# Optimization experiments

Measured on AMD Instinct MI355X. Metric: run time of the kernel, lower is better.

## Reference

```python
import jax, jax.numpy as jnp
import numpy as np

B, LQ, LM = 8, 128, 512
Q_SIZE, M_SIZE, H_SIZE = 512, 512, 256
MASKED_VALUE = -1e24


def setup_inputs() -> dict:
    key = jax.random.key(0)
    ks = jax.random.split(key, 8)
    query = jax.random.normal(ks[0], (B, LQ, Q_SIZE), dtype=jnp.float32)
    memory = jax.random.normal(ks[1], (B, LM, M_SIZE), dtype=jnp.float32)
    mask = jax.random.randint(ks[2], (B, LM), 0, 2).astype(bool)
    s_q = 1.0 / np.sqrt(Q_SIZE)
    s_m = 1.0 / np.sqrt(M_SIZE)
    s_h = 1.0 / np.sqrt(H_SIZE)
    Wq = jax.random.uniform(ks[3], (Q_SIZE, H_SIZE), jnp.float32, -s_q, s_q)
    bq = jax.random.uniform(ks[4], (H_SIZE,), jnp.float32, -s_q, s_q)
    Wm = jax.random.uniform(ks[5], (M_SIZE, H_SIZE), jnp.float32, -s_m, s_m)
    v = jax.random.uniform(ks[6], (H_SIZE,), jnp.float32, -s_h, s_h)
    return {"query": query, "memory": memory, "mask": mask,
            "Wq": Wq, "bq": bq, "Wm": Wm, "v": v}


def reference(query, memory, mask, Wq, bq, Wm, v):
    # mlp (Bahdanau) attention; key defaults to memory
    q_proj = jnp.einsum('bqd,dh->bqh', query, Wq) + bq      # [B,Lq,H]
    k_proj = jnp.einsum('bmd,dh->bmh', memory, Wm)          # [B,Lm,H]
    hidden = jnp.tanh(q_proj[:, :, None, :] + k_proj[:, None, :, :])  # [B,Lq,Lm,H]
    attn = jnp.einsum('bqmh,h->bqm', hidden, v)             # [B,Lq,Lm]
    attn = jnp.where(mask[:, None, :], MASKED_VALUE, attn)
    weights = jax.nn.softmax(attn, axis=-1)
    weighted_memory = jnp.einsum('bqm,bmd->bqd', weights, memory)
    return weighted_memory, weights
```

## Files before the change

### kernel.cpp

```cpp
#include <hip/hip_runtime.h>
#include <hip/hip_bf16.h>

#define B_   8
#define LQ_  128
#define LM_  512
#define D_   512
#define H_   256
#define MASKVAL -1e24f
#define PRESCALE 2.88539008177792681f

typedef __attribute__((ext_vector_type(8))) short bf16x8;
typedef __attribute__((ext_vector_type(4))) float f32x4;

__device__ __forceinline__ ushort f2bf(float x) {
    return __builtin_bit_cast(ushort, __float2bfloat16(x));
}

#define PBM 32
#define PBN 32
#define PBK 64
#define PLDK 88

__global__ __launch_bounds__(256) void proj_mfma(
    const float* __restrict__ query, const float* __restrict__ memory,
    const float* __restrict__ Wq, const float* __restrict__ Wm,
    const float* __restrict__ bq,
    float* __restrict__ qp, float* __restrict__ kp)
{
    __shared__ ushort As[PBM][PLDK];
    __shared__ ushort Bs[PBN][PLDK];

    const int mtile = blockIdx.x % 160;
    const int ntile = blockIdx.x / 160;
    const int n0 = ntile * PBN;
    const bool is_q = (mtile < 32);
    const float* X = is_q ? (query  + (size_t)mtile * PBM * D_)
                          : (memory + (size_t)(mtile - 32) * PBM * D_);
    const float* W = is_q ? Wq : Wm;
    float* out     = is_q ? (qp + (size_t)mtile * PBM * H_)
                          : (kp + (size_t)(mtile - 32) * PBM * H_);

    const int t = threadIdx.x;
    const int lane = t & 63, w = t >> 6;
    const int wm = (w & 1) * 16, wn = (w >> 1) * 16;

    const int ar  = t >> 4;
    const int akq = t & 15;

    const int frow = lane & 15;
    const int fkof = (lane >> 4) * 8;

    f32x4 acc = {0.f, 0.f, 0.f, 0.f};

    for (int k0 = 0; k0 < D_; k0 += PBK) {
#pragma unroll
        for (int p = 0; p < 2; ++p) {
            const int row = ar + p * 16;
            const float4 x4 = *(const float4*)(X + (size_t)row * D_ + k0 + akq * 4);
            ushort4 u4;
            u4.x = f2bf(x4.x); u4.y = f2bf(x4.y); u4.z = f2bf(x4.z); u4.w = f2bf(x4.w);
            *(ushort4*)&As[row][akq * 4] = u4;
        }
#pragma unroll
        for (int p = 0; p < 2; ++p) {
            const int L  = t + p * 256;
            const int kk = L >> 3;
            const int f4 = L & 7;
            const float4 w4 = *(const float4*)(W + (size_t)(k0 + kk) * H_ + n0 + f4 * 4);
            Bs[f4 * 4 + 0][kk] = f2bf(w4.x);
            Bs[f4 * 4 + 1][kk] = f2bf(w4.y);
            Bs[f4 * 4 + 2][kk] = f2bf(w4.z);
            Bs[f4 * 4 + 3][kk] = f2bf(w4.w);
        }
        __syncthreads();
#pragma unroll
        for (int ks = 0; ks < PBK; ks += 32) {
            bf16x8 a = *(const bf16x8*)&As[wm + frow][ks + fkof];
            bf16x8 b = *(const bf16x8*)&Bs[wn + frow][ks + fkof];
            acc = __builtin_amdgcn_mfma_f32_16x16x32_bf16(a, b, acc, 0, 0, 0);
        }
        __syncthreads();
    }

    const int col  = n0 + wn + (lane & 15);
    const int rloc = wm + (lane >> 4) * 4;
    const float bias = is_q ? bq[col] : 0.0f;
#pragma unroll
    for (int r = 0; r < 4; ++r)
        out[(size_t)(rloc + r) * H_ + col] =
            __builtin_amdgcn_exp2f((acc[r] + bias) * PRESCALE);
}

#define PIN4(X) asm volatile("" : "+v"(X.x), "+v"(X.y), "+v"(X.z), "+v"(X.w))

__global__ __launch_bounds__(512, 2) void attn_kernel(
    const float* __restrict__ qp,
    const float* __restrict__ kp,
    const float* __restrict__ memory,
    const int*   __restrict__ mask,
    const float* __restrict__ v,
    float* __restrict__ out_wm,
    float* __restrict__ out_w)
{
    __shared__ float scores[4][512];
    __shared__ int   mlist[512];
    __shared__ int   nact_sh;
    __shared__ float sv_sh;

    const int t = threadIdx.x;
    const int b  = blockIdx.x & 7;
    const int qg = blockIdx.x >> 3;
    const int rowbase = b * LQ_ + qg * 4;
    const int w = t >> 6, lane = t & 63;

    ((float4*)&scores[0][0])[t] = make_float4(MASKVAL, MASKVAL, MASKVAL, MASKVAL);

    if (w == 6) {
        const float4 c = *(const float4*)(v + lane * 4);
        float s = c.x + c.y + c.z + c.w;
        s += __shfl_xor(s, 1);  s += __shfl_xor(s, 2);
        s += __shfl_xor(s, 4);  s += __shfl_xor(s, 8);
        s += __shfl_xor(s, 16); s += __shfl_xor(s, 32);
        if (lane == 0) sv_sh = s;
    }
    if (w == 7) {
        unsigned base = 0;
        for (int it = 0; it < 8; ++it) {
            int m = it * 64 + lane;
            int act = (mask[b * 512 + m] == 0);
            unsigned long long bal = __ballot(act);
            if (act) {
                int pos = __popcll(bal & ((1ull << lane) - 1ull));
                mlist[base + pos] = m;
            }
            base += __popcll(bal);
        }
        if (lane == 0) nact_sh = (int)base;
    }

    const int lane16 = lane & 15, mg = lane >> 4;
    const int col = lane16 * 4;
    float4 qreg[4][4], vreg[4];
#pragma unroll
    for (int j = 0; j < 4; ++j) {
        vreg[j] = *(const float4*)(v + j * 64 + col);
        PIN4(vreg[j]);
    }
#pragma unroll
    for (int q = 0; q < 4; ++q)
#pragma unroll
        for (int j = 0; j < 4; ++j) {
            qreg[q][j] = *(const float4*)(qp + (size_t)(rowbase + q) * 256 + j * 64 + col);
            PIN4(qreg[q][j]);
        }

    __syncthreads();
    const int nact = nact_sh;
    const float sv = sv_sh;

    if (nact > 0) {
        const float* kbase = kp + (size_t)b * 512 * 256 + col;
        int i = w * 4 + mg;
        const int last = nact - 1;
        int mcur = mlist[i <= last ? i : last];
        float4 k0 = *(const float4*)(kbase + (size_t)mcur * 256);
        float4 k1 = *(const float4*)(kbase + (size_t)mcur * 256 + 64);
        float4 k2 = *(const float4*)(kbase + (size_t)mcur * 256 + 128);
        float4 k3 = *(const float4*)(kbase + (size_t)mcur * 256 + 192);
        const int nit = (nact + 31) >> 5;
        for (int it = 0; it < nit; ++it) {
            const int inext = i + 32;
            const int mnext = mlist[inext <= last ? inext : last];
            float4 n0, n1, n2, n3;
            if (it + 1 < nit) {
                n0 = *(const float4*)(kbase + (size_t)mnext * 256);
                n1 = *(const float4*)(kbase + (size_t)mnext * 256 + 64);
                n2 = *(const float4*)(kbase + (size_t)mnext * 256 + 128);
                n3 = *(const float4*)(kbase + (size_t)mnext * 256 + 192);
            }
            float acc0 = 0.f, acc1 = 0.f, acc2 = 0.f, acc3 = 0.f;
#define COMP(J, C) { \
            const float kk = k##J.C, vv = vreg[J].C; \
            acc0 = fmaf(vv, __builtin_amdgcn_rcpf(fmaf(qreg[0][J].C, kk, 1.f)), acc0); \
            acc1 = fmaf(vv, __builtin_amdgcn_rcpf(fmaf(qreg[1][J].C, kk, 1.f)), acc1); \
            acc2 = fmaf(vv, __builtin_amdgcn_rcpf(fmaf(qreg[2][J].C, kk, 1.f)), acc2); \
            acc3 = fmaf(vv, __builtin_amdgcn_rcpf(fmaf(qreg[3][J].C, kk, 1.f)), acc3); }
            COMP(0, x) COMP(0, y) COMP(0, z) COMP(0, w)
            COMP(1, x) COMP(1, y) COMP(1, z) COMP(1, w)
            COMP(2, x) COMP(2, y) COMP(2, z) COMP(2, w)
            COMP(3, x) COMP(3, y) COMP(3, z) COMP(3, w)
#undef COMP
#define RED(X) X += __shfl_xor(X, 1); X += __shfl_xor(X, 2); \
               X += __shfl_xor(X, 4); X += __shfl_xor(X, 8);
            RED(acc0) RED(acc1) RED(acc2) RED(acc3)
#undef RED
            if (lane16 == 0 && i < nact) {
                scores[0][mcur] = fmaf(-2.f, acc0, sv);
                scores[1][mcur] = fmaf(-2.f, acc1, sv);
                scores[2][mcur] = fmaf(-2.f, acc2, sv);
                scores[3][mcur] = fmaf(-2.f, acc3, sv);
            }
            i = inext; mcur = mnext;
            k0 = n0; k1 = n1; k2 = n2; k3 = n3;
        }
    }
    __syncthreads();

    if (w < 4) {
        const int q = w, row = rowbase + q;
        float s[8], e[8];
        float mx = -INFINITY;
#pragma unroll
        for (int k = 0; k < 8; ++k) { s[k] = scores[q][lane + 64 * k]; mx = fmaxf(mx, s[k]); }
#pragma unroll
        for (int off = 32; off >= 1; off >>= 1) mx = fmaxf(mx, __shfl_xor(mx, off));
        float sum = 0.0f;
#pragma unroll
        for (int k = 0; k < 8; ++k) {
            e[k] = __builtin_amdgcn_exp2f((s[k] - mx) * 1.44269504088896341f);
            sum += e[k];
        }
#pragma unroll
        for (int off = 32; off >= 1; off >>= 1) sum += __shfl_xor(sum, off);
        float rs = __builtin_amdgcn_rcpf(sum);
#pragma unroll
        for (int k = 0; k < 8; ++k) {
            float wt = e[k] * rs;
            scores[q][lane + 64 * k] = wt;
            out_w[(size_t)row * 512 + lane + 64 * k] = wt;
        }
    }
    __syncthreads();

    {
        const int d = t;
        const float* mb = memory + (size_t)b * 512 * 512 + d;
        float a0 = 0.f, a1 = 0.f, a2 = 0.f, a3 = 0.f;
        int i = 0;
        for (; i + 4 <= nact; i += 4) {
            const int m0 = mlist[i], m1 = mlist[i + 1], m2 = mlist[i + 2], m3 = mlist[i + 3];
            const float v0 = mb[(size_t)m0 * 512];
            const float v1 = mb[(size_t)m1 * 512];
            const float v2 = mb[(size_t)m2 * 512];
            const float v3 = mb[(size_t)m3 * 512];
            a0 = fmaf(scores[0][m3], v3, fmaf(scores[0][m2], v2, fmaf(scores[0][m1], v1, fmaf(scores[0][m0], v0, a0))));
            a1 = fmaf(scores[1][m3], v3, fmaf(scores[1][m2], v2, fmaf(scores[1][m1], v1, fmaf(scores[1][m0], v0, a1))));
            a2 = fmaf(scores[2][m3], v3, fmaf(scores[2][m2], v2, fmaf(scores[2][m1], v1, fmaf(scores[2][m0], v0, a2))));
            a3 = fmaf(scores[3][m3], v3, fmaf(scores[3][m2], v2, fmaf(scores[3][m1], v1, fmaf(scores[3][m0], v0, a3))));
        }
        for (; i < nact; ++i) {
            const int m0 = mlist[i];
            const float v0 = mb[(size_t)m0 * 512];
            a0 = fmaf(scores[0][m0], v0, a0);
            a1 = fmaf(scores[1][m0], v0, a1);
            a2 = fmaf(scores[2][m0], v0, a2);
            a3 = fmaf(scores[3][m0], v0, a3);
        }
        out_wm[(size_t)(rowbase + 0) * 512 + d] = a0;
        out_wm[(size_t)(rowbase + 1) * 512 + d] = a1;
        out_wm[(size_t)(rowbase + 2) * 512 + d] = a2;
        out_wm[(size_t)(rowbase + 3) * 512 + d] = a3;
    }
}

extern "C" void kernel_launch(void* const* d_in, const int* in_sizes, int n_in,
                              void* d_out, int out_size, void* d_ws, size_t ws_size,
                              hipStream_t stream) {
    const float* query  = (const float*)d_in[0];
    const float* memory = (const float*)d_in[1];
    const int*   mask   = (const int*)  d_in[2];
    const float* Wq     = (const float*)d_in[3];
    const float* bq     = (const float*)d_in[4];
    const float* Wm     = (const float*)d_in[5];
    const float* v      = (const float*)d_in[6];

    float* out_wm = (float*)d_out;
    float* out_w  = out_wm + (size_t)B_ * LQ_ * D_;

    float* qp = (float*)d_ws;
    float* kp = qp + (size_t)B_ * LQ_ * H_;

    hipLaunchKernelGGL(proj_mfma, dim3(160 * (H_ / PBN)), dim3(256), 0, stream,
                       query, memory, Wq, Wm, bq, qp, kp);
    hipLaunchKernelGGL(attn_kernel, dim3(B_ * (LQ_ / 4)), dim3(512), 0, stream,
                       qp, kp, memory, mask, v, out_wm, out_w);
}
```

Measured before the change: 48.12 us.

## Split fused attention kernel into separate scores, softmax and PV kernels

Breaks the single attention kernel into three launches: a scores kernel that handles two query rows per block (twice as many blocks) and writes raw scores to a workspace, a softmax kernel that applies the mask and normalises, and a PV kernel with 1024-thread blocks that reads the normalised weights from global memory. The aim is more blocks and higher occupancy in the scores phase, plus lower register pressure and a wider PV phase. In exchange it adds two kernel launches and a global round trip for the score and weight matrices. It also recomputes the active-column list in the PV kernel.

```diff
diff --git a/kernel.cpp b/kernel.cpp
--- a/kernel.cpp
+++ b/kernel.cpp
@@ -43,10 +43,8 @@
     const int t = threadIdx.x;
     const int lane = t & 63, w = t >> 6;
     const int wm = (w & 1) * 16, wn = (w >> 1) * 16;
-
     const int ar  = t >> 4;
     const int akq = t & 15;
-
     const int frow = lane & 15;
     const int fkof = (lane >> 4) * 8;
 
@@ -93,16 +91,13 @@
 
 #define PIN4(X) asm volatile("" : "+v"(X.x), "+v"(X.y), "+v"(X.z), "+v"(X.w))
 
-__global__ __launch_bounds__(512, 2) void attn_kernel(
+__global__ __launch_bounds__(512, 4) void scores_kernel(
     const float* __restrict__ qp,
     const float* __restrict__ kp,
-    const float* __restrict__ memory,
     const int*   __restrict__ mask,
     const float* __restrict__ v,
-    float* __restrict__ out_wm,
-    float* __restrict__ out_w)
+    float* __restrict__ sc)
 {
-    __shared__ float scores[4][512];
     __shared__ int   mlist[512];
     __shared__ int   nact_sh;
     __shared__ float sv_sh;
@@ -110,10 +105,10 @@
     const int t = threadIdx.x;
     const int b  = blockIdx.x & 7;
     const int qg = blockIdx.x >> 3;
-    const int rowbase = b * LQ_ + qg * 4;
+    const int rowbase = b * LQ_ + qg * 2;
     const int w = t >> 6, lane = t & 63;
-
-    ((float4*)&scores[0][0])[t] = make_float4(MASKVAL, MASKVAL, MASKVAL, MASKVAL);
+    const int lane16 = lane & 15, mg = lane >> 4;
+    const int col = lane16 * 4;
 
     if (w == 6) {
         const float4 c = *(const float4*)(v + lane * 4);
@@ -138,16 +133,14 @@
         if (lane == 0) nact_sh = (int)base;
     }
 
-    const int lane16 = lane & 15, mg = lane >> 4;
-    const int col = lane16 * 4;
-    float4 qreg[4][4], vreg[4];
+    float4 qreg[2][4], vreg[4];
 #pragma unroll
     for (int j = 0; j < 4; ++j) {
         vreg[j] = *(const float4*)(v + j * 64 + col);
         PIN4(vreg[j]);
     }
 #pragma unroll
-    for (int q = 0; q < 4; ++q)
+    for (int q = 0; q < 2; ++q)
 #pragma unroll
         for (int j = 0; j < 4; ++j) {
             qreg[q][j] = *(const float4*)(qp + (size_t)(rowbase + q) * 256 + j * 64 + col);
@@ -157,110 +150,147 @@
     __syncthreads();
     const int nact = nact_sh;
     const float sv = sv_sh;
-
-    if (nact > 0) {
-        const float* kbase = kp + (size_t)b * 512 * 256 + col;
-        int i = w * 4 + mg;
-        const int last = nact - 1;
-        int mcur = mlist[i <= last ? i : last];
-        float4 k0 = *(const float4*)(kbase + (size_t)mcur * 256);
-        float4 k1 = *(const float4*)(kbase + (size_t)mcur * 256 + 64);
-        float4 k2 = *(const float4*)(kbase + (size_t)mcur * 256 + 128);
-        float4 k3 = *(const float4*)(kbase + (size_t)mcur * 256 + 192);
-        const int nit = (nact + 31) >> 5;
-        for (int it = 0; it < nit; ++it) {
-            const int inext = i + 32;
-            const int mnext = mlist[inext <= last ? inext : last];
-            float4 n0, n1, n2, n3;
-            if (it + 1 < nit) {
-                n0 = *(const float4*)(kbase + (size_t)mnext * 256);
-                n1 = *(const float4*)(kbase + (size_t)mnext * 256 + 64);
-                n2 = *(const float4*)(kbase + (size_t)mnext * 256 + 128);
-                n3 = *(const float4*)(kbase + (size_t)mnext * 256 + 192);
-            }
-            float acc0 = 0.f, acc1 = 0.f, acc2 = 0.f, acc3 = 0.f;
+    if (nact == 0) return;
+
+    const float* kbase = kp + (size_t)b * 512 * 256 + col;
+    int i = w * 4 + mg;
+    const int last = nact - 1;
+    int mcur = mlist[i <= last ? i : last];
+    float4 k0 = *(const float4*)(kbase + (size_t)mcur * 256);
+    float4 k1 = *(const float4*)(kbase + (size_t)mcur * 256 + 64);
+    float4 k2 = *(const float4*)(kbase + (size_t)mcur * 256 + 128);
+    float4 k3 = *(const float4*)(kbase + (size_t)mcur * 256 + 192);
+    const int nit = (nact + 31) >> 5;
+    for (int it = 0; it < nit; ++it) {
+        const int inext = i + 32;
+        const int mnext = mlist[inext <= last ? inext : last];
+        float4 n0, n1, n2, n3;
+        if (it + 1 < nit) {
+            n0 = *(const float4*)(kbase + (size_t)mnext * 256);
+            n1 = *(const float4*)(kbase + (size_t)mnext * 256 + 64);
+            n2 = *(const float4*)(kbase + (size_t)mnext * 256 + 128);
+            n3 = *(const float4*)(kbase + (size_t)mnext * 256 + 192);
+        }
+        float acc0 = 0.f, acc1 = 0.f;
 #define COMP(J, C) { \
-            const float kk = k##J.C, vv = vreg[J].C; \
-            acc0 = fmaf(vv, __builtin_amdgcn_rcpf(fmaf(qreg[0][J].C, kk, 1.f)), acc0); \
-            acc1 = fmaf(vv, __builtin_amdgcn_rcpf(fmaf(qreg[1][J].C, kk, 1.f)), acc1); \
-            acc2 = fmaf(vv, __builtin_amdgcn_rcpf(fmaf(qreg[2][J].C, kk, 1.f)), acc2); \
-            acc3 = fmaf(vv, __builtin_amdgcn_rcpf(fmaf(qreg[3][J].C, kk, 1.f)), acc3); }
-            COMP(0, x) COMP(0, y) COMP(0, z) COMP(0, w)
-            COMP(1, x) COMP(1, y) COMP(1, z) COMP(1, w)
-            COMP(2, x) COMP(2, y) COMP(2, z) COMP(2, w)
-            COMP(3, x) COMP(3, y) COMP(3, z) COMP(3, w)
+        const float kk = k##J.C, vv = vreg[J].C; \
+        acc0 = fmaf(vv, __builtin_amdgcn_rcpf(fmaf(qreg[0][J].C, kk, 1.f)), acc0); \
+        acc1 = fmaf(vv, __builtin_amdgcn_rcpf(fmaf(qreg[1][J].C, kk, 1.f)), acc1); }
+        COMP(0, x) COMP(0, y) COMP(0, z) COMP(0, w)
+        COMP(1, x) COMP(1, y) COMP(1, z) COMP(1, w)
+        COMP(2, x) COMP(2, y) COMP(2, z) COMP(2, w)
+        COMP(3, x) COMP(3, y) COMP(3, z) COMP(3, w)
 #undef COMP
 #define RED(X) X += __shfl_xor(X, 1); X += __shfl_xor(X, 2); \
                X += __shfl_xor(X, 4); X += __shfl_xor(X, 8);
-            RED(acc0) RED(acc1) RED(acc2) RED(acc3)
+        RED(acc0) RED(acc1)
 #undef RED
-            if (lane16 == 0 && i < nact) {
-                scores[0][mcur] = fmaf(-2.f, acc0, sv);
-                scores[1][mcur] = fmaf(-2.f, acc1, sv);
-                scores[2][mcur] = fmaf(-2.f, acc2, sv);
-                scores[3][mcur] = fmaf(-2.f, acc3, sv);
+        if (lane16 == 0 && i < nact) {
+            sc[(size_t)(rowbase + 0) * 512 + mcur] = fmaf(-2.f, acc0, sv);
+            sc[(size_t)(rowbase + 1) * 512 + mcur] = fmaf(-2.f, acc1, sv);
+        }
+        i = inext; mcur = mnext;
+        k0 = n0; k1 = n1; k2 = n2; k3 = n3;
+    }
+}
+
+__global__ __launch_bounds__(256) void softmax_kernel(
+    const float* __restrict__ sc,
+    const int*   __restrict__ mask,
+    float* __restrict__ out_w)
+{
+    const int t = threadIdx.x;
+    const int b  = blockIdx.x & 7;
+    const int qg = blockIdx.x >> 3;
+    const int row = b * LQ_ + qg * 4 + (t >> 6);
+    const int lane = t & 63;
+
+    float s[8], e[8];
+    float mx = -INFINITY;
+#pragma unroll
+    for (int k = 0; k < 8; ++k) {
+        const int m = lane + 64 * k;
+        const int msk = mask[b * 512 + m];
+        s[k] = msk ? MASKVAL : sc[(size_t)row * 512 + m];
+        mx = fmaxf(mx, s[k]);
+    }
+#pragma unroll
+    for (int off = 32; off >= 1; off >>= 1) mx = fmaxf(mx, __shfl_xor(mx, off));
+    float sum = 0.0f;
+#pragma unroll
+    for (int k = 0; k < 8; ++k) {
+        e[k] = __builtin_amdgcn_exp2f((s[k] - mx) * 1.44269504088896341f);
+        sum += e[k];
+    }
+#pragma unroll
+    for (int off = 32; off >= 1; off >>= 1) sum += __shfl_xor(sum, off);
+    const float rs = __builtin_amdgcn_rcpf(sum);
+#pragma unroll
+    for (int k = 0; k < 8; ++k)
+        out_w[(size_t)row * 512 + lane + 64 * k] = e[k] * rs;
+}
+
+__global__ __launch_bounds__(1024, 4) void pv_kernel(
+    const float* __restrict__ wts,
+    const float* __restrict__ memory,
+    const int*   __restrict__ mask,
+    float* __restrict__ out_wm)
+{
+    __shared__ int mlist[512];
+    __shared__ int nact_sh;
+
+    const int t = threadIdx.x;
+    const int b  = blockIdx.x & 7;
+    const int qg = blockIdx.x >> 3;
+    const int rowbase = b * LQ_ + qg * 4;
+    const int w = t >> 6, lane = t & 63;
+
+    if (w == 15) {
+        unsigned base = 0;
+        for (int it = 0; it < 8; ++it) {
+            int m = it * 64 + lane;
+            int act = (mask[b * 512 + m] == 0);
+            unsigned long long bal = __ballot(act);
+            if (act) {
+                int pos = __popcll(bal & ((1ull << lane) - 1ull));
+                mlist[base + pos] = m;
             }
-            i = inext; mcur = mnext;
-            k0 = n0; k1 = n1; k2 = n2; k3 = n3;
-        }
+            base += __popcll(bal);
+        }
+        if (lane == 0) nact_sh = (int)base;
     }
     __syncthreads();
-
-    if (w < 4) {
-        const int q = w, row = rowbase + q;
-        float s[8], e[8];
-        float mx = -INFINITY;
-#pragma unroll
-        for (int k = 0; k < 8; ++k) { s[k] = scores[q][lane + 64 * k]; mx = fmaxf(mx, s[k]); }
-#pragma unroll
-        for (int off = 32; off >= 1; off >>= 1) mx = fmaxf(mx, __shfl_xor(mx, off));
-        float sum = 0.0f;
-#pragma unroll
-        for (int k = 0; k < 8; ++k) {
-            e[k] = __builtin_amdgcn_exp2f((s[k] - mx) * 1.44269504088896341f);
-            sum += e[k];
-        }
-#pragma unroll
-        for (int off = 32; off >= 1; off >>= 1) sum += __shfl_xor(sum, off);
-        float rs = __builtin_amdgcn_rcpf(sum);
-#pragma unroll
-        for (int k = 0; k < 8; ++k) {
-            float wt = e[k] * rs;
-            scores[q][lane + 64 * k] = wt;
-            out_w[(size_t)row * 512 + lane + 64 * k] = wt;
-        }
-    }
-    __syncthreads();
-
-    {
-        const int d = t;
-        const float* mb = memory + (size_t)b * 512 * 512 + d;
-        float a0 = 0.f, a1 = 0.f, a2 = 0.f, a3 = 0.f;
-        int i = 0;
-        for (; i + 4 <= nact; i += 4) {
-            const int m0 = mlist[i], m1 = mlist[i + 1], m2 = mlist[i + 2], m3 = mlist[i + 3];
-            const float v0 = mb[(size_t)m0 * 512];
-            const float v1 = mb[(size_t)m1 * 512];
-            const float v2 = mb[(size_t)m2 * 512];
-            const float v3 = mb[(size_t)m3 * 512];
-            a0 = fmaf(scores[0][m3], v3, fmaf(scores[0][m2], v2, fmaf(scores[0][m1], v1, fmaf(scores[0][m0], v0, a0))));
-            a1 = fmaf(scores[1][m3], v3, fmaf(scores[1][m2], v2, fmaf(scores[1][m1], v1, fmaf(scores[1][m0], v0, a1))));
-            a2 = fmaf(scores[2][m3], v3, fmaf(scores[2][m2], v2, fmaf(scores[2][m1], v1, fmaf(scores[2][m0], v0, a2))));
-            a3 = fmaf(scores[3][m3], v3, fmaf(scores[3][m2], v2, fmaf(scores[3][m1], v1, fmaf(scores[3][m0], v0, a3))));
-        }
-        for (; i < nact; ++i) {
-            const int m0 = mlist[i];
-            const float v0 = mb[(size_t)m0 * 512];
-            a0 = fmaf(scores[0][m0], v0, a0);
-            a1 = fmaf(scores[1][m0], v0, a1);
-            a2 = fmaf(scores[2][m0], v0, a2);
-            a3 = fmaf(scores[3][m0], v0, a3);
-        }
-        out_wm[(size_t)(rowbase + 0) * 512 + d] = a0;
-        out_wm[(size_t)(rowbase + 1) * 512 + d] = a1;
-        out_wm[(size_t)(rowbase + 2) * 512 + d] = a2;
-        out_wm[(size_t)(rowbase + 3) * 512 + d] = a3;
-    }
+    const int nact = nact_sh;
+
+    const int d  = t & 511;
+    const int qh = t >> 9;
+    const float* mb = memory + (size_t)b * 512 * 512 + d;
+    const float* w0r = wts + (size_t)(rowbase + qh * 2 + 0) * 512;
+    const float* w1r = wts + (size_t)(rowbase + qh * 2 + 1) * 512;
+    float a0 = 0.f, a1 = 0.f;
+    int i = 0;
+    for (; i + 4 <= nact; i += 4) {
+        const int m0 = __builtin_amdgcn_readfirstlane(mlist[i]);
+        const int m1 = __builtin_amdgcn_readfirstlane(mlist[i + 1]);
+        const int m2 = __builtin_amdgcn_readfirstlane(mlist[i + 2]);
+        const int m3 = __builtin_amdgcn_readfirstlane(mlist[i + 3]);
+        const float v0 = mb[(size_t)m0 * 512];
+        const float v1 = mb[(size_t)m1 * 512];
+        const float v2 = mb[(size_t)m2 * 512];
+        const float v3 = mb[(size_t)m3 * 512];
+        const float s00 = w0r[m0], s01 = w0r[m1], s02 = w0r[m2], s03 = w0r[m3];
+        const float s10 = w1r[m0], s11 = w1r[m1], s12 = w1r[m2], s13 = w1r[m3];
+        a0 = fmaf(s03, v3, fmaf(s02, v2, fmaf(s01, v1, fmaf(s00, v0, a0))));
+        a1 = fmaf(s13, v3, fmaf(s12, v2, fmaf(s11, v1, fmaf(s10, v0, a1))));
+    }
+    for (; i < nact; ++i) {
+        const int m0 = __builtin_amdgcn_readfirstlane(mlist[i]);
+        const float v0 = mb[(size_t)m0 * 512];
+        a0 = fmaf(w0r[m0], v0, a0);
+        a1 = fmaf(w1r[m0], v0, a1);
+    }
+    out_wm[(size_t)(rowbase + qh * 2 + 0) * 512 + d] = a0;
+    out_wm[(size_t)(rowbase + qh * 2 + 1) * 512 + d] = a1;
 }
 
 extern "C" void kernel_launch(void* const* d_in, const int* in_sizes, int n_in,
@@ -279,9 +309,14 @@
 
     float* qp = (float*)d_ws;
     float* kp = qp + (size_t)B_ * LQ_ * H_;
+    float* sc = kp + (size_t)B_ * LM_ * H_;
 
     hipLaunchKernelGGL(proj_mfma, dim3(160 * (H_ / PBN)), dim3(256), 0, stream,
                        query, memory, Wq, Wm, bq, qp, kp);
-    hipLaunchKernelGGL(attn_kernel, dim3(B_ * (LQ_ / 4)), dim3(512), 0, stream,
-                       qp, kp, memory, mask, v, out_wm, out_w);
-}
+    hipLaunchKernelGGL(scores_kernel, dim3(B_ * (LQ_ / 2)), dim3(512), 0, stream,
+                       qp, kp, mask, v, sc);
+    hipLaunchKernelGGL(softmax_kernel, dim3(B_ * (LQ_ / 4)), dim3(256), 0, stream,
+                       sc, mask, out_w);
+    hipLaunchKernelGGL(pv_kernel, dim3(B_ * (LQ_ / 4)), dim3(1024), 0, stream,
+                       out_w, memory, mask, out_wm);
+}
```

Result: slower. 68.13 us (+41.6%).
